# Performance work log

Hardware: AMD Instinct MI355X
Metric: run time of the kernel (lower is better)

## Reference

```python
import jax, jax.numpy as jnp
import numpy as np

EPS = 1e-6
D = 512      # embedding_dim
M = 4        # n_modules
B = 4        # batch
S = 128      # seq_len
K = 32       # stack_size
STEPS = 16   # max_steps (ACT)
SCALE = D ** (-0.5)


def _clin(zr, zi, Wr, Wi, sub):
    # complex linear: (Wr + i Wi)(zr + i zi), torch Linear convention y = x @ W.T
    yr = jnp.einsum(sub, zr, Wr) - jnp.einsum(sub, zi, Wi)
    yi = jnp.einsum(sub, zi, Wr) + jnp.einsum(sub, zr, Wi)
    return yr, yi


def forward_fn(x_real, x_imag, Wl_r, Wl_i, Wq_r, Wq_i, Wk_r, Wk_i, Wv_r, Wv_i,
               ln_scale, ln_shift, mod_bias, gate_mask,
               score_w, score_b, conf_w, conf_b, halt_w, halt_b,
               ctrl_w, ctrl_b, st_score_w, st_score_b, st_conf_w, st_conf_b):
    mem0 = jnp.zeros((B, K, 2 * D), x_real.dtype)
    ptr0 = jnp.zeros((B, K), x_real.dtype).at[:, 0].set(1.0)
    acc0 = jnp.zeros((B, S, 2 * D), x_real.dtype)
    rem0 = jnp.ones((B,), x_real.dtype)

    def step(carry, _):
        sr, si, mem, ptr, acc, rem = carry
        # ComplexAttentionBlock (all M modules vectorized on axis m)
        cr = 0.5 * x_real + 0.5 * sr
        ci = 0.5 * x_imag + 0.5 * si
        zr, zi = _clin(cr, ci, Wl_r, Wl_i, 'bsd,mod->bmso')   # [B,M,S,D]
        # ComplexLayerNorm (magnitude LN, unbiased var as torch.var default)
        mag = jnp.sqrt(zr * zr + zi * zi) + EPS
        mean = mag.mean(-1, keepdims=True)
        var = mag.var(-1, keepdims=True, ddof=1)
        nm = (mag - mean) / jnp.sqrt(var + EPS)
        nm = nm * ln_scale[None, :, None, :] + ln_shift[None, :, None, :]
        ph = jnp.arctan2(zi, zr)
        zr = nm * jnp.cos(ph)
        zi = nm * jnp.sin(ph)
        # ModReLU
        nrm = jnp.sqrt(zr * zr + zi * zi) + EPS
        sc = jax.nn.relu(nrm + mod_bias[None, :, None, :]) / nrm
        zr = zr * sc
        zi = zi * sc
        # ComplexAttention over concatenated real/imag q,k
        sub = 'bmsd,mod->bmso'
        qr, qi = _clin(zr, zi, Wq_r, Wq_i, sub)
        kr, ki = _clin(zr, zi, Wk_r, Wk_i, sub)
        vr, vi = _clin(zr, zi, Wv_r, Wv_i, sub)
        qf = jnp.concatenate([qr, qi], -1)   # [B,M,S,2D]
        kf = jnp.concatenate([kr, ki], -1)
        attn = jax.nn.softmax(jnp.einsum('bmse,bmte->bmst', qf, kf) * SCALE, axis=-1)
        ar = jnp.einsum('bmst,bmtd->bmsd', attn, vr)
        ai = jnp.einsum('bmst,bmtd->bmsd', attn, vi)
        # SigmoidGatingMask
        g = jax.nn.sigmoid(gate_mask)[None, :, None, :]
        pr = ar * g
        pi = ai * g
        flat = jnp.concatenate([pr, pi], -1)  # [B,M,S,2D]
        score = jnp.einsum('bmse,me->bms', flat, score_w) + score_b[None, :, None]
        conf = jax.nn.sigmoid(jnp.einsum('bmse,me->bms', flat, conf_w) + conf_b[None, :, None])
        halt = jnp.einsum('bmse,me->bms', flat, halt_w) + halt_b[None, :, None]
        # DifferentiableStack on seq-pooled broadcast state
        flat_in = jnp.concatenate([sr.mean(1), si.mean(1)], -1)  # [B,2D]
        control = jax.nn.softmax(flat_in @ ctrl_w + ctrl_b, axis=-1)  # [B,3]
        push, pop, noop = control[:, 0:1], control[:, 1:2], control[:, 2:3]
        ptr_up = jnp.roll(ptr, 1, axis=1)
        ptr_dn = jnp.roll(ptr, -1, axis=1)
        new_ptr = push * ptr_up + pop * ptr_dn + noop * ptr
        new_ptr = new_ptr / (new_ptr.sum(1, keepdims=True) + EPS)
        wmask = push * ptr_up                                   # [B,K]
        new_mem = wmask[..., None] * flat_in[:, None, :] + mem * (1.0 - wmask[..., None])
        read = (new_mem * new_ptr[..., None]).sum(1)            # [B,2D]
        sp_r, sp_i = read[:, :D], read[:, D:]
        st_sc = read @ st_score_w + st_score_b[0]               # [B]
        st_cf = jax.nn.sigmoid(read @ st_conf_w + st_conf_b[0])
        # combine M block proposals + stack proposal via score*confidence softmax
        all_pr = jnp.concatenate([pr, jnp.broadcast_to(sp_r[:, None, None, :], (B, 1, S, D))], 1)
        all_pi = jnp.concatenate([pi, jnp.broadcast_to(sp_i[:, None, None, :], (B, 1, S, D))], 1)
        all_sc = jnp.concatenate([score, jnp.broadcast_to(st_sc[:, None, None], (B, 1, S))], 1)
        all_cf = jnp.concatenate([conf, jnp.broadcast_to(st_cf[:, None, None], (B, 1, S))], 1)
        w = jax.nn.softmax(all_sc * all_cf, axis=1)[..., None]  # [B,M+1,S,1]
        new_sr = (w * all_pr).sum(1)
        new_si = (w * all_pi).sum(1)
        # ACT halting accumulation
        p = jax.nn.sigmoid(halt).mean(axis=(1, 2))              # [B]
        acc = acc + (p * rem)[:, None, None] * jnp.concatenate([new_sr, new_si], -1)
        rem = rem * (1.0 - p)
        return (new_sr, new_si, new_mem, new_ptr, acc, rem), None

    carry, _ = jax.lax.scan(step, (x_real, x_imag, mem0, ptr0, acc0, rem0), None, length=STEPS)
    sr, si, _, _, acc, rem = carry
    # add ACT remainder weight on final state
    out = acc + rem[:, None, None] * jnp.concatenate([sr, si], -1)
    return out  # [B,S,2D] real/imag concat


def setup_inputs() -> dict:
    key = jax.random.key(0)
    ks = jax.random.split(key, 24)
    w = 1.0 / np.sqrt(D)
    h = 0.02
    inp = {
        'x_real': jax.random.normal(ks[0], (B, S, D), jnp.float32),
        'x_imag': jax.random.normal(ks[1], (B, S, D), jnp.float32),
        'Wl_r': jax.random.normal(ks[2], (M, D, D), jnp.float32) * w,
        'Wl_i': jax.random.normal(ks[3], (M, D, D), jnp.float32) * w,
        'Wq_r': jax.random.normal(ks[4], (M, D, D), jnp.float32) * w,
        'Wq_i': jax.random.normal(ks[5], (M, D, D), jnp.float32) * w,
        'Wk_r': jax.random.normal(ks[6], (M, D, D), jnp.float32) * w,
        'Wk_i': jax.random.normal(ks[7], (M, D, D), jnp.float32) * w,
        'Wv_r': jax.random.normal(ks[8], (M, D, D), jnp.float32) * w,
        'Wv_i': jax.random.normal(ks[9], (M, D, D), jnp.float32) * w,
        'ln_scale': jnp.ones((M, D), jnp.float32),
        'ln_shift': jnp.zeros((M, D), jnp.float32),
        'mod_bias': jnp.zeros((M, D), jnp.float32),
        'gate_mask': jnp.ones((M, D), jnp.float32),
        'score_w': jax.random.normal(ks[10], (M, 2 * D), jnp.float32) * h,
        'score_b': jnp.zeros((M,), jnp.float32),
        'conf_w': jax.random.normal(ks[11], (M, 2 * D), jnp.float32) * h,
        'conf_b': jnp.zeros((M,), jnp.float32),
        'halt_w': jax.random.normal(ks[12], (M, 2 * D), jnp.float32) * h,
        'halt_b': jnp.full((M,), -4.0, jnp.float32),  # nn.init.constant_(halt_head.bias, -4.0)
        'ctrl_w': jax.random.normal(ks[13], (2 * D, 3), jnp.float32) * h,
        'ctrl_b': jnp.zeros((3,), jnp.float32),
        'st_score_w': jax.random.normal(ks[14], (2 * D,), jnp.float32) * h,
        'st_score_b': jnp.zeros((1,), jnp.float32),
        'st_conf_w': jax.random.normal(ks[15], (2 * D,), jnp.float32) * h,
        'st_conf_b': jnp.zeros((1,), jnp.float32),
    }
    return inp


def reference(x_real, x_imag, Wl_r, Wl_i, Wq_r, Wq_i, Wk_r, Wk_i, Wv_r, Wv_i,
              ln_scale, ln_shift, mod_bias, gate_mask,
              score_w, score_b, conf_w, conf_b, halt_w, halt_b,
              ctrl_w, ctrl_b, st_score_w, st_score_b, st_conf_w, st_conf_b):
    return forward_fn(x_real, x_imag, Wl_r, Wl_i, Wq_r, Wq_i, Wk_r, Wk_i, Wv_r, Wv_i,
                      ln_scale, ln_shift, mod_bias, gate_mask,
                      score_w, score_b, conf_w, conf_b, halt_w, halt_b,
                      ctrl_w, ctrl_b, st_score_w, st_score_b, st_conf_w, st_conf_b)
```

## Files before the change

kernel.cpp:

```cpp
#include <hip/hip_runtime.h>

#define DD 512
#define MM 4
#define BB 4
#define SS 128
#define KK 32
#define NSTEPS 16
#define EPSF 1e-6f
#define SCALEF 0.04419417382415922f

typedef unsigned short u16;
typedef __bf16 bf16x8 __attribute__((ext_vector_type(8)));
typedef u16 u16x8 __attribute__((ext_vector_type(8)));
typedef float f32x16 __attribute__((ext_vector_type(16)));
typedef unsigned int u32x4 __attribute__((ext_vector_type(4)));

__device__ inline void split_bf16(float x, u16& h, u16& l) {
  __bf16 hb = (__bf16)x;
  float hf = (float)hb;
  __bf16 lb = (__bf16)(x - hf);
  h = __builtin_bit_cast(u16, hb);
  l = __builtin_bit_cast(u16, lb);
}

__global__ void k_convw(const float* __restrict__ src, u16* __restrict__ dst) {
  int idx = blockIdx.x * 256 + threadIdx.x;
  int row = idx >> 9, k = idx & 511;
  u16 h, l;
  split_bf16(src[idx], h, l);
  dst[(size_t)row * 1024 + k] = h;
  dst[(size_t)row * 1024 + 512 + k] = l;
}

__global__ void k_convt(const float* __restrict__ src, u16* __restrict__ dst) {
  __shared__ float tile[64][65];
  int m = blockIdx.z;
  int o0 = blockIdx.y * 64, d0 = blockIdx.x * 64;
  int tid = threadIdx.x;
  int g = tid >> 6, lane = tid & 63;
#pragma unroll
  for (int i = 0; i < 16; i++) {
    int o_l = g * 16 + i;
// ... 93 lines not shown
    ctrl[0] = e0 / s; ctrl[1] = e1 / s; ctrl[2] = e2 / s;
    stacc[b * 2] = 0.f; stacc[b * 2 + 1] = 0.f;
  }
  __syncthreads();
  if (tid < KK) {
    float up = optr[(tid + KK - 1) & (KK - 1)];
    float dn = optr[(tid + 1) & (KK - 1)];
    float cu = optr[tid];
    nptr_s[tid] = ctrl[0] * up + ctrl[1] * dn + ctrl[2] * cu;
    wm_s[tid] = ctrl[0] * up;
  }
  __syncthreads();
  if (tid == 0) {
    float s = 0.f;
    for (int k = 0; k < KK; k++) s += nptr_s[k];
    normf = 1.f / (s + EPSF);
  }
  __syncthreads();
  if (tid < KK) {
    float np = nptr_s[tid] * normf;
    ptrv[b * KK + tid] = np;
    nptrg[b * KK + tid] = np;
    wmg[b * KK + tid] = wm_s[tid];
  }
}

#define LSTR 72

__global__ __launch_bounds__(256) void k_gemm_mfma(
    const u16* __restrict__ Ar, const u16* __restrict__ Ai,
    const u16* __restrict__ Wr, const u16* __restrict__ Wi,
    float* __restrict__ Cr, float* __restrict__ Ci) {
  __shared__ u16 sAr[64][LSTR], sAi[64][LSTR], sWr[64][LSTR], sWi[64][LSTR];
  int m = blockIdx.z;
  int row_blk = blockIdx.y * 64, o_blk = blockIdx.x * 64;
  int tid = threadIdx.x;

  int lrow = tid >> 3, lk8 = (tid & 7) << 3;
  size_t arow0 = (size_t)(row_blk + lrow), arow1 = arow0 + 32;
  size_t wrow0 = (size_t)m * DD + o_blk + lrow, wrow1 = wrow0 + 32;

  int wave = tid >> 6, lane = tid & 63;
  int wrow = (wave >> 1) * 32, wcol = (wave & 1) * 32;
  int l31 = lane & 31, khalf = (lane >> 5) * 8;

  f32x16 accP, accN, accI;
  for (int i = 0; i < 16; i++) { accP[i] = 0.f; accN[i] = 0.f; accI[i] = 0.f; }

  u16x8 g0 = *(const u16x8*)&Ar[arow0 * 1024 + lk8];
  u16x8 g1 = *(const u16x8*)&Ar[arow1 * 1024 + lk8];
  u16x8 g2 = *(const u16x8*)&Ai[arow0 * 1024 + lk8];
  u16x8 g3 = *(const u16x8*)&Ai[arow1 * 1024 + lk8];
  u16x8 g4 = *(const u16x8*)&Wr[wrow0 * 1024 + lk8];
  u16x8 g5 = *(const u16x8*)&Wr[wrow1 * 1024 + lk8];
  u16x8 g6 = *(const u16x8*)&Wi[wrow0 * 1024 + lk8];
  u16x8 g7 = *(const u16x8*)&Wi[wrow1 * 1024 + lk8];

  for (int it = 0; it < 24; ++it) {
    __syncthreads();
    *(u16x8*)&sAr[lrow][lk8] = g0;
    *(u16x8*)&sAr[lrow + 32][lk8] = g1;
    *(u16x8*)&sAi[lrow][lk8] = g2;
    *(u16x8*)&sAi[lrow + 32][lk8] = g3;
    *(u16x8*)&sWr[lrow][lk8] = g4;
    *(u16x8*)&sWr[lrow + 32][lk8] = g5;
    *(u16x8*)&sWi[lrow][lk8] = g6;
    *(u16x8*)&sWi[lrow + 32][lk8] = g7;
    u16x8 n0, n1, n2, n3, n4, n5, n6, n7;
    if (it < 23) {
      int it2 = it + 1, seg = it2 >> 3, k0 = (it2 & 7) * 64;
      int aofs = (seg == 1) ? 512 : 0, wofs = (seg == 2) ? 512 : 0;
      n0 = *(const u16x8*)&Ar[arow0 * 1024 + aofs + k0 + lk8];
      n1 = *(const u16x8*)&Ar[arow1 * 1024 + aofs + k0 + lk8];
      n2 = *(const u16x8*)&Ai[arow0 * 1024 + aofs + k0 + lk8];
      n3 = *(const u16x8*)&Ai[arow1 * 1024 + aofs + k0 + lk8];
      n4 = *(const u16x8*)&Wr[wrow0 * 1024 + wofs + k0 + lk8];
      n5 = *(const u16x8*)&Wr[wrow1 * 1024 + wofs + k0 + lk8];
      n6 = *(const u16x8*)&Wi[wrow0 * 1024 + wofs + k0 + lk8];
      n7 = *(const u16x8*)&Wi[wrow1 * 1024 + wofs + k0 + lk8];
    }
    __syncthreads();
#pragma unroll
    for (int kk = 0; kk < 64; kk += 16) {
      bf16x8 fAr = *(const bf16x8*)&sAr[wrow + l31][kk + khalf];
      bf16x8 fAi = *(const bf16x8*)&sAi[wrow + l31][kk + khalf];
      bf16x8 fWr = *(const bf16x8*)&sWr[wcol + l31][kk + khalf];
      bf16x8 fWi = *(const bf16x8*)&sWi[wcol + l31][kk + khalf];
      accP = __builtin_amdgcn_mfma_f32_32x32x16_bf16(fAr, fWr, accP, 0, 0, 0);
      accN = __builtin_amdgcn_mfma_f32_32x32x16_bf16(fAi, fWi, accN, 0, 0, 0);
      accI = __builtin_amdgcn_mfma_f32_32x32x16_bf16(fAi, fWr, accI, 0, 0, 0);
      accI = __builtin_amdgcn_mfma_f32_32x32x16_bf16(fAr, fWi, accI, 0, 0, 0);
    }
    if (it < 23) {
      g0 = n0; g1 = n1; g2 = n2; g3 = n3; g4 = n4; g5 = n5; g6 = n6; g7 = n7;
    }
  }

  int o = o_blk + wcol + l31;
#pragma unroll
  for (int reg = 0; reg < 16; reg++) {
    int r_in = (reg & 3) + 8 * (reg >> 2) + 4 * (lane >> 5);
    int gr = row_blk + wrow + r_in;
    int b = gr >> 7, s = gr & (SS - 1);
    size_t crow = (size_t)((b * MM + m) * SS + s);
    Cr[crow * DD + o] = accP[reg] - accN[reg];
    Ci[crow * DD + o] = accI[reg];
  }
}

__global__ __launch_bounds__(256) void k_gemm_g(
    const u16* __restrict__ Ar, const u16* __restrict__ Ai,
    const u16* __restrict__ Wr, const u16* __restrict__ Wi,
    float* __restrict__ Hr, float* __restrict__ Hi) {
  __shared__ u16 sAr[64][LSTR], sAi[64][LSTR], sWr[64][LSTR], sWi[64][LSTR];
  int m = blockIdx.z;
  int row_blk = blockIdx.y * 64, o_blk = blockIdx.x * 64;
  int tid = threadIdx.x;

  int lrow = tid >> 3, lk8 = (tid & 7) << 3;
  size_t arow0 = (size_t)(m * 512 + row_blk + lrow), arow1 = arow0 + 32;
  size_t wrow0 = (size_t)(m * 512 + o_blk + lrow), wrow1 = wrow0 + 32;

  int wave = tid >> 6, lane = tid & 63;
  int wrow = (wave >> 1) * 32, wcol = (wave & 1) * 32;
  int l31 = lane & 31, khalf = (lane >> 5) * 8;

  f32x16 accP, accN, accI;
  for (int i = 0; i < 16; i++) { accP[i] = 0.f; accN[i] = 0.f; accI[i] = 0.f; }

  u16x8 g0 = *(const u16x8*)&Ar[arow0 * 1024 + lk8];
  u16x8 g1 = *(const u16x8*)&Ar[arow1 * 1024 + lk8];
  u16x8 g2 = *(const u16x8*)&Ai[arow0 * 1024 + lk8];
  u16x8 g3 = *(const u16x8*)&Ai[arow1 * 1024 + lk8];
  u16x8 g4 = *(const u16x8*)&Wr[wrow0 * 1024 + lk8];
  u16x8 g5 = *(const u16x8*)&Wr[wrow1 * 1024 + lk8];
  u16x8 g6 = *(const u16x8*)&Wi[wrow0 * 1024 + lk8];
  u16x8 g7 = *(const u16x8*)&Wi[wrow1 * 1024 + lk8];

  for (int it = 0; it < 24; ++it) {
    __syncthreads();
    *(u16x8*)&sAr[lrow][lk8] = g0;
    *(u16x8*)&sAr[lrow + 32][lk8] = g1;
    *(u16x8*)&sAi[lrow][lk8] = g2;
    *(u16x8*)&sAi[lrow + 32][lk8] = g3;
    *(u16x8*)&sWr[lrow][lk8] = g4;
    *(u16x8*)&sWr[lrow + 32][lk8] = g5;
    *(u16x8*)&sWi[lrow][lk8] = g6;
    *(u16x8*)&sWi[lrow + 32][lk8] = g7;
    u16x8 n0, n1, n2, n3, n4, n5, n6, n7;
    if (it < 23) {
      int it2 = it + 1, seg = it2 >> 3, k0 = (it2 & 7) * 64;
      int aofs = (seg == 1) ? 512 : 0, wofs = (seg == 2) ? 512 : 0;
      n0 = *(const u16x8*)&Ar[arow0 * 1024 + aofs + k0 + lk8];
      n1 = *(const u16x8*)&Ar[arow1 * 1024 + aofs + k0 + lk8];
      n2 = *(const u16x8*)&Ai[arow0 * 1024 + aofs + k0 + lk8];
      n3 = *(const u16x8*)&Ai[arow1 * 1024 + aofs + k0 + lk8];
      n4 = *(const u16x8*)&Wr[wrow0 * 1024 + wofs + k0 + lk8];
      n5 = *(const u16x8*)&Wr[wrow1 * 1024 + wofs + k0 + lk8];
      n6 = *(const u16x8*)&Wi[wrow0 * 1024 + wofs + k0 + lk8];
      n7 = *(const u16x8*)&Wi[wrow1 * 1024 + wofs + k0 + lk8];
    }
    __syncthreads();
#pragma unroll
    for (int kk = 0; kk < 64; kk += 16) {
      bf16x8 fAr = *(const bf16x8*)&sAr[wrow + l31][kk + khalf];
      bf16x8 fAi = *(const bf16x8*)&sAi[wrow + l31][kk + khalf];
      bf16x8 fWr = *(const bf16x8*)&sWr[wcol + l31][kk + khalf];
      bf16x8 fWi = *(const bf16x8*)&sWi[wcol + l31][kk + khalf];
      u32x4 t = __builtin_bit_cast(u32x4, fAi) ^ 0x80008000u;
      bf16x8 nAi = __builtin_bit_cast(bf16x8, t);
      accP = __builtin_amdgcn_mfma_f32_32x32x16_bf16(fAr, fWr, accP, 0, 0, 0);
      accN = __builtin_amdgcn_mfma_f32_32x32x16_bf16(fAi, fWi, accN, 0, 0, 0);
      accI = __builtin_amdgcn_mfma_f32_32x32x16_bf16(fAr, fWi, accI, 0, 0, 0);
      accI = __builtin_amdgcn_mfma_f32_32x32x16_bf16(nAi, fWr, accI, 0, 0, 0);
    }
    if (it < 23) {
      g0 = n0; g1 = n1; g2 = n2; g3 = n3; g4 = n4; g5 = n5; g6 = n6; g7 = n7;
    }
  }

  int o = o_blk + wcol + l31;
#pragma unroll
  for (int reg = 0; reg < 16; reg++) {
    int r_in = (reg & 3) + 8 * (reg >> 2) + 4 * (lane >> 5);
    int gr = row_blk + wrow + r_in;
    size_t crow = (size_t)(m * 512 + gr);
    Hr[crow * DD + o] = accP[reg] + accN[reg];
    Hi[crow * DD + o] = accI[reg];
  }
}

__global__ __launch_bounds__(256) void k_gemm_qkv(
    const u16* __restrict__ Ar, const u16* __restrict__ Ai,
    const u16* __restrict__ wbf, size_t WSLOT,
    u16* __restrict__ qbr, u16* __restrict__ qbi,
    u16* __restrict__ vbr, u16* __restrict__ vbi) {
  __shared__ u16 sAr[64][LSTR], sAi[64][LSTR], sWr[64][LSTR], sWi[64][LSTR];
  int zid = blockIdx.z;
  int m = zid >> 1, w = zid & 1;
  int slot = (w == 0) ? 8 : 6;
  const u16* Wr = wbf + (size_t)slot * WSLOT;
  const u16* Wi = Wr + WSLOT;
  int row_blk = blockIdx.y * 64, o_blk = blockIdx.x * 64;
  int tid = threadIdx.x;

  int lrow = tid >> 3, lk8 = (tid & 7) << 3;
  int gr0 = row_blk + lrow, gr1 = gr0 + 32;
  size_t arow0 = (size_t)(((gr0 >> 7) * MM + m) * SS + (gr0 & (SS - 1)));
  size_t arow1 = (size_t)(((gr1 >> 7) * MM + m) * SS + (gr1 & (SS - 1)));
  size_t wrow0 = (size_t)m * DD + o_blk + lrow, wrow1 = wrow0 + 32;

  int wave = tid >> 6, lane = tid & 63;
  int wrow = (wave >> 1) * 32, wcol = (wave & 1) * 32;
  int l31 = lane & 31, khalf = (lane >> 5) * 8;

  f32x16 accP, accN, accI;
  for (int i = 0; i < 16; i++) { accP[i] = 0.f; accN[i] = 0.f; accI[i] = 0.f; }

  u16x8 g0 = *(const u16x8*)&Ar[arow0 * 1024 + lk8];
  u16x8 g1 = *(const u16x8*)&Ar[arow1 * 1024 + lk8];
  u16x8 g2 = *(const u16x8*)&Ai[arow0 * 1024 + lk8];
  u16x8 g3 = *(const u16x8*)&Ai[arow1 * 1024 + lk8];
  u16x8 g4 = *(const u16x8*)&Wr[wrow0 * 1024 + lk8];
  u16x8 g5 = *(const u16x8*)&Wr[wrow1 * 1024 + lk8];
  u16x8 g6 = *(const u16x8*)&Wi[wrow0 * 1024 + lk8];
  u16x8 g7 = *(const u16x8*)&Wi[wrow1 * 1024 + lk8];

  for (int it = 0; it < 24; ++it) {
    __syncthreads();
    *(u16x8*)&sAr[lrow][lk8] = g0;
    *(u16x8*)&sAr[lrow + 32][lk8] = g1;
    *(u16x8*)&sAi[lrow][lk8] = g2;
    *(u16x8*)&sAi[lrow + 32][lk8] = g3;
    *(u16x8*)&sWr[lrow][lk8] = g4;
    *(u16x8*)&sWr[lrow + 32][lk8] = g5;
    *(u16x8*)&sWi[lrow][lk8] = g6;
    *(u16x8*)&sWi[lrow + 32][lk8] = g7;
    u16x8 n0, n1, n2, n3, n4, n5, n6, n7;
    if (it < 23) {
      int it2 = it + 1, seg = it2 >> 3, k0 = (it2 & 7) * 64;
      int aofs = (seg == 1) ? 512 : 0, wofs = (seg == 2) ? 512 : 0;
      n0 = *(const u16x8*)&Ar[arow0 * 1024 + aofs + k0 + lk8];
      n1 = *(const u16x8*)&Ar[arow1 * 1024 + aofs + k0 + lk8];
      n2 = *(const u16x8*)&Ai[arow0 * 1024 + aofs + k0 + lk8];
      n3 = *(const u16x8*)&Ai[arow1 * 1024 + aofs + k0 + lk8];
      n4 = *(const u16x8*)&Wr[wrow0 * 1024 + wofs + k0 + lk8];
      n5 = *(const u16x8*)&Wr[wrow1 * 1024 + wofs + k0 + lk8];
      n6 = *(const u16x8*)&Wi[wrow0 * 1024 + wofs + k0 + lk8];
      n7 = *(const u16x8*)&Wi[wrow1 * 1024 + wofs + k0 + lk8];
    }
    __syncthreads();
#pragma unroll
    for (int kk = 0; kk < 64; kk += 16) {
      bf16x8 fAr = *(const bf16x8*)&sAr[wrow + l31][kk + khalf];
      bf16x8 fAi = *(const bf16x8*)&sAi[wrow + l31][kk + khalf];
      bf16x8 fWr = *(const bf16x8*)&sWr[wcol + l31][kk + khalf];
      bf16x8 fWi = *(const bf16x8*)&sWi[wcol + l31][kk + khalf];
      accP = __builtin_amdgcn_mfma_f32_32x32x16_bf16(fAr, fWr, accP, 0, 0, 0);
      accN = __builtin_amdgcn_mfma_f32_32x32x16_bf16(fAi, fWi, accN, 0, 0, 0);
      accI = __builtin_amdgcn_mfma_f32_32x32x16_bf16(fAi, fWr, accI, 0, 0, 0);
      accI = __builtin_amdgcn_mfma_f32_32x32x16_bf16(fAr, fWi, accI, 0, 0, 0);
    }
    if (it < 23) {
      g0 = n0; g1 = n1; g2 = n2; g3 = n3; g4 = n4; g5 = n5; g6 = n6; g7 = n7;
    }
  }

  u16* Cr = (w == 0) ? qbr : vbr;
  u16* Ci = (w == 0) ? qbi : vbi;
  int o = o_blk + wcol + l31;
#pragma unroll
  for (int reg = 0; reg < 16; reg++) {
    int r_in = (reg & 3) + 8 * (reg >> 2) + 4 * (lane >> 5);
    int gr = row_blk + wrow + r_in;
    int b = gr >> 7, s = gr & (SS - 1);
    size_t crow = (size_t)((b * MM + m) * SS + s);
    u16 h, l;
    split_bf16(accP[reg] - accN[reg], h, l);
    Cr[crow * 1024 + o] = h;
    Cr[crow * 1024 + 512 + o] = l;
    split_bf16(accI[reg], h, l);
    Ci[crow * 1024 + o] = h;
    Ci[crow * 1024 + 512 + o] = l;
  }
}

__global__ __launch_bounds__(256) void k_scores_sm(
    const u16* __restrict__ Q_r, const u16* __restrict__ Q_i,
    const u16* __restrict__ K_r, const u16* __restrict__ K_i,
    u16* __restrict__ Pb) {
  __shared__ __align__(16) char smem[55296];
  u16 (*sQr)[LSTR] = (u16(*)[LSTR])smem;
  u16 (*sQi)[LSTR] = (u16(*)[LSTR])(smem + 9216);
  u16 (*sKr)[LSTR] = (u16(*)[LSTR])(smem + 18432);
  u16 (*sKi)[LSTR] = (u16(*)[LSTR])(smem + 36864);
  float (*stile)[132] = (float(*)[132])smem;

  int bm = blockIdx.z;
  int s_blk = blockIdx.y * 64;
  int tid = threadIdx.x;
  int lrow = tid >> 3, lk8 = (tid & 7) << 3;
  size_t qrow0 = (size_t)(bm * SS + s_blk + lrow), qrow1 = qrow0 + 32;
  size_t krow = (size_t)(bm * SS + lrow);

  int wave = tid >> 6, lane = tid & 63;
  int srow_w = (wave & 1) * 32;
  int tcol_w = (wave >> 1) * 64;
  int l31 = lane & 31, khalf = (lane >> 5) * 8;

  f32x16 acc0, acc1;
  for (int i = 0; i < 16; i++) { acc0[i] = 0.f; acc1[i] = 0.f; }

  for (int it = 0; it < 24; ++it) {
    int seg = it >> 3, k0 = (it & 7) * 64;
    int qofs = (seg == 1) ? 512 : 0;
    int kofs = (seg == 2) ? 512 : 0;
    u16x8 q0 = *(const u16x8*)&Q_r[qrow0 * 1024 + qofs + k0 + lk8];
    u16x8 q1 = *(const u16x8*)&Q_r[qrow1 * 1024 + qofs + k0 + lk8];
    u16x8 q2 = *(const u16x8*)&Q_i[qrow0 * 1024 + qofs + k0 + lk8];
    u16x8 q3 = *(const u16x8*)&Q_i[qrow1 * 1024 + qofs + k0 + lk8];
    u16x8 kr0 = *(const u16x8*)&K_r[(krow + 0) * 1024 + kofs + k0 + lk8];
    u16x8 kr1 = *(const u16x8*)&K_r[(krow + 32) * 1024 + kofs + k0 + lk8];
    u16x8 kr2 = *(const u16x8*)&K_r[(krow + 64) * 1024 + kofs + k0 + lk8];
    u16x8 kr3 = *(const u16x8*)&K_r[(krow + 96) * 1024 + kofs + k0 + lk8];
    u16x8 ki0 = *(const u16x8*)&K_i[(krow + 0) * 1024 + kofs + k0 + lk8];
    u16x8 ki1 = *(const u16x8*)&K_i[(krow + 32) * 1024 + kofs + k0 + lk8];
    u16x8 ki2 = *(const u16x8*)&K_i[(krow + 64) * 1024 + kofs + k0 + lk8];
    u16x8 ki3 = *(const u16x8*)&K_i[(krow + 96) * 1024 + kofs + k0 + lk8];
    __syncthreads();
    *(u16x8*)&sQr[lrow][lk8] = q0;
    *(u16x8*)&sQr[lrow + 32][lk8] = q1;
    *(u16x8*)&sQi[lrow][lk8] = q2;
    *(u16x8*)&sQi[lrow + 32][lk8] = q3;
    *(u16x8*)&sKr[lrow][lk8] = kr0;
    *(u16x8*)&sKr[lrow + 32][lk8] = kr1;
    *(u16x8*)&sKr[lrow + 64][lk8] = kr2;
    *(u16x8*)&sKr[lrow + 96][lk8] = kr3;
    *(u16x8*)&sKi[lrow][lk8] = ki0;
    *(u16x8*)&sKi[lrow + 32][lk8] = ki1;
    *(u16x8*)&sKi[lrow + 64][lk8] = ki2;
    *(u16x8*)&sKi[lrow + 96][lk8] = ki3;
    __syncthreads();
#pragma unroll
    for (int kk = 0; kk < 64; kk += 16) {
      bf16x8 fQr = *(const bf16x8*)&sQr[srow_w + l31][kk + khalf];
      bf16x8 fQi = *(const bf16x8*)&sQi[srow_w + l31][kk + khalf];
      bf16x8 fKr0 = *(const bf16x8*)&sKr[tcol_w + l31][kk + khalf];
      bf16x8 fKr1 = *(const bf16x8*)&sKr[tcol_w + 32 + l31][kk + khalf];
      bf16x8 fKi0 = *(const bf16x8*)&sKi[tcol_w + l31][kk + khalf];
      bf16x8 fKi1 = *(const bf16x8*)&sKi[tcol_w + 32 + l31][kk + khalf];
      acc0 = __builtin_amdgcn_mfma_f32_32x32x16_bf16(fQr, fKr0, acc0, 0, 0, 0);
      acc0 = __builtin_amdgcn_mfma_f32_32x32x16_bf16(fQi, fKi0, acc0, 0, 0, 0);
      acc1 = __builtin_amdgcn_mfma_f32_32x32x16_bf16(fQr, fKr1, acc1, 0, 0, 0);
      acc1 = __builtin_amdgcn_mfma_f32_32x32x16_bf16(fQi, fKi1, acc1, 0, 0, 0);
    }
  }

  __syncthreads();
#pragma unroll
  for (int reg = 0; reg < 16; reg++) {
    int r = srow_w + (reg & 3) + 8 * (reg >> 2) + 4 * (lane >> 5);
    stile[r][tcol_w + l31] = acc0[reg] * SCALEF;
    stile[r][tcol_w + 32 + l31] = acc1[reg] * SCALEF;
  }
  __syncthreads();
  int row = tid >> 2;
  int quarter = tid & 3;
  float mx = -3.4e38f;
#pragma unroll
  for (int j = 0; j < 32; j++) mx = fmaxf(mx, stile[row][quarter * 32 + j]);
  mx = fmaxf(mx, __shfl_xor(mx, 1));
  mx = fmaxf(mx, __shfl_xor(mx, 2));
  float ev[32];
  float sum = 0.f;
#pragma unroll
  for (int j = 0; j < 32; j++) {
    ev[j] = expf(stile[row][quarter * 32 + j] - mx);
    sum += ev[j];
  }
  sum += __shfl_xor(sum, 1);
  sum += __shfl_xor(sum, 2);
  float inv = 1.f / sum;
  size_t prow = (size_t)(bm * SS + s_blk + row) * 256;
#pragma unroll
  for (int j = 0; j < 32; j++) {
    int c = quarter * 32 + j;
    u16 h, l;
// ... 72 lines not shown
    float vR = accR[reg] * g, vI = accI[reg] * g;
    pr[crow * DD + d] = vR;
    pi[crow * DD + d] = vI;
    float ps = vR * swr + vI * swi;
    float pc = vR * cwr + vI * cwi;
    float ph = vR * hwr + vI * hwi;
#pragma unroll
    for (int off = 1; off < 32; off <<= 1) {
      ps += __shfl_xor(ps, off);
      pc += __shfl_xor(pc, off);
      ph += __shfl_xor(ph, off);
    }
    if (l31 == 0) {
      atomicAdd(&scorev[crow], ps);
      atomicAdd(&confv[crow], pc);
      atomicAdd(&haltv[crow], ph);
    }
  }
}

__global__ void k_lnphase(const float* __restrict__ zr, const float* __restrict__ zi,
                          const float* __restrict__ ln_scale, const float* __restrict__ ln_shift,
                          const float* __restrict__ mod_bias,
                          u16* __restrict__ zbr, u16* __restrict__ zbi) {
  int row = blockIdx.x;
  int m = (row >> 7) & (MM - 1);
  int tid = threadIdx.x;
  size_t base = (size_t)row * DD;
  float zrv[4], ziv[4], rv[4];
  float sum = 0.f, sumsq = 0.f;
#pragma unroll
  for (int i = 0; i < 4; i++) {
    int o = tid + i * 128;
    float a = zr[base + o], bv = zi[base + o];
    zrv[i] = a; ziv[i] = bv;
    float r = sqrtf(a * a + bv * bv);
    rv[i] = r;
    float mg = r + EPSF;
    sum += mg;
    sumsq += mg * mg;
  }
  __shared__ float rs[128], rq[128];
  rs[tid] = sum; rq[tid] = sumsq;
  __syncthreads();
  for (int off = 64; off > 0; off >>= 1) {
    if (tid < off) { rs[tid] += rs[tid + off]; rq[tid] += rq[tid + off]; }
    __syncthreads();
  }
  float mean = rs[0] * (1.0f / DD);
  float var = (rq[0] - (float)DD * mean * mean) * (1.0f / (DD - 1));
  float inv = 1.0f / sqrtf(var + EPSF);
#pragma unroll
  for (int i = 0; i < 4; i++) {
    int o = tid + i * 128;
    float mg = rv[i] + EPSF;
    float nm = (mg - mean) * inv * ln_scale[m * DD + o] + ln_shift[m * DD + o];
    float r = rv[i];
    float cosp, sinp;
    if (r > 0.f) { cosp = zrv[i] / r; sinp = ziv[i] / r; }
    else { cosp = 1.f; sinp = 0.f; }
    float z1r = nm * cosp, z1i = nm * sinp;
    float nrm = sqrtf(z1r * z1r + z1i * z1i) + EPSF;
    float sc = fmaxf(nrm + mod_bias[m * DD + o], 0.f) / nrm;
    u16 h, l;
    split_bf16(z1r * sc, h, l);
    zbr[(size_t)row * 1024 + o] = h;
    zbr[(size_t)row * 1024 + 512 + o] = l;
// ... 134 lines not shown

extern "C" void kernel_launch(void* const* d_in, const int* in_sizes, int n_in,
                              void* d_out, int out_size, void* d_ws, size_t ws_size,
                              hipStream_t stream) {
  const float* xr = (const float*)d_in[0];
  const float* xi = (const float*)d_in[1];
  const float* Wl_r = (const float*)d_in[2];
  const float* Wl_i = (const float*)d_in[3];
  const float* Wq_r = (const float*)d_in[4];
  const float* Wq_i = (const float*)d_in[5];
  const float* Wk_r = (const float*)d_in[6];
  const float* Wk_i = (const float*)d_in[7];
  const float* Wv_r = (const float*)d_in[8];
  const float* Wv_i = (const float*)d_in[9];
  const float* ln_scale = (const float*)d_in[10];
  const float* ln_shift = (const float*)d_in[11];
  const float* mod_bias = (const float*)d_in[12];
  const float* gate_mask = (const float*)d_in[13];
  const float* score_w = (const float*)d_in[14];
  const float* score_b = (const float*)d_in[15];
  const float* conf_w = (const float*)d_in[16];
  const float* conf_b = (const float*)d_in[17];
  const float* halt_w = (const float*)d_in[18];
  const float* halt_b = (const float*)d_in[19];
  const float* ctrl_w = (const float*)d_in[20];
  const float* ctrl_b = (const float*)d_in[21];
  const float* st_score_w = (const float*)d_in[22];
  const float* st_score_b = (const float*)d_in[23];
  const float* st_conf_w = (const float*)d_in[24];
  const float* st_conf_b = (const float*)d_in[25];
  float* out = (float*)d_out;

  const int BSD = BB * SS * DD;
  const int BMSD = BB * MM * SS * DD;
  const size_t WSLOT = (size_t)MM * DD * 1024;

  char* pc = (char*)d_ws;
  float* sr = (float*)pc; pc += (size_t)BSD * 4;
  float* si = (float*)pc; pc += (size_t)BSD * 4;
  float* zr = (float*)pc; pc += (size_t)BMSD * 4;
  float* zi = (float*)pc; pc += (size_t)BMSD * 4;
  float* prb = (float*)pc; pc += (size_t)BMSD * 4;
  float* pib = (float*)pc; pc += (size_t)BMSD * 4;
  float* scorev = (float*)pc; pc += (size_t)BB * MM * SS * 4;
  float* confv = (float*)pc; pc += (size_t)BB * MM * SS * 4;
  float* haltv = (float*)pc; pc += (size_t)BB * MM * SS * 4;
  float* flat = (float*)pc; pc += (size_t)BB * 2 * DD * 4;
  float* stacc = (float*)pc; pc += 64;
  float* nptrg = (float*)pc; pc += (size_t)BB * KK * 4;
  float* wmg = (float*)pc; pc += (size_t)BB * KK * 4;
  float* memv = (float*)pc; pc += (size_t)BB * KK * 2 * DD * 4;
  float* ptrv = (float*)pc; pc += (size_t)BB * KK * 4;
  float* readv = (float*)pc; pc += (size_t)BB * 2 * DD * 4;
  float* stv = (float*)pc; pc += (size_t)2 * BB * 4;
  float* accb = (float*)pc; pc += (size_t)BB * SS * 2 * DD * 4;
  float* rem = (float*)pc; pc += (size_t)BB * 4;
  float* coeff = (float*)pc; pc += (size_t)BB * 4;
  u16* crbf = (u16*)pc; pc += (size_t)BB * SS * 1024 * 2;
  u16* cibf = (u16*)pc; pc += (size_t)BB * SS * 1024 * 2;
  u16* zbr = (u16*)pc; pc += (size_t)BB * MM * SS * 1024 * 2;
  u16* zbi = (u16*)pc; pc += (size_t)BB * MM * SS * 1024 * 2;
  u16* qbr = (u16*)pc; pc += (size_t)BB * MM * SS * 1024 * 2;
  u16* qbi = (u16*)pc; pc += (size_t)BB * MM * SS * 1024 * 2;
  u16* vbr = (u16*)pc; pc += (size_t)BB * MM * SS * 1024 * 2;
  u16* vbi = (u16*)pc; pc += (size_t)BB * MM * SS * 1024 * 2;
  u16* Pb  = (u16*)pc; pc += (size_t)BB * MM * SS * 256 * 2;
  u16* wbf = (u16*)pc; pc += 10 * WSLOT * 2;
  u16* wqtr = (u16*)pc; pc += WSLOT * 2;
  u16* wqti = (u16*)pc; pc += WSLOT * 2;
  u16* wktr = (u16*)pc; pc += WSLOT * 2;
  u16* wkti = (u16*)pc; pc += WSLOT * 2;
  float* hfr = (float*)pc; pc += (size_t)MM * DD * DD * 4;
  float* hfi = (float*)pc; pc += (size_t)MM * DD * DD * 4;

  k_convw<<<4096, 256, 0, stream>>>(Wl_r, wbf + 0 * WSLOT);
  k_convw<<<4096, 256, 0, stream>>>(Wl_i, wbf + 1 * WSLOT);
  k_convw<<<4096, 256, 0, stream>>>(Wv_r, wbf + 6 * WSLOT);
  k_convw<<<4096, 256, 0, stream>>>(Wv_i, wbf + 7 * WSLOT);

  dim3 tgrid(8, 8, 4);
  k_convt<<<tgrid, 256, 0, stream>>>(Wq_r, wqtr);
  k_convt<<<tgrid, 256, 0, stream>>>(Wq_i, wqti);
  k_convt<<<tgrid, 256, 0, stream>>>(Wk_r, wktr);
  k_convt<<<tgrid, 256, 0, stream>>>(Wk_i, wkti);

  dim3 hgrid(8, 8, 4);
  k_gemm_g<<<hgrid, 256, 0, stream>>>(wktr, wkti, wqtr, wqti, hfr, hfi);
  k_convw<<<4096, 256, 0, stream>>>(hfr, wbf + 8 * WSLOT);
  k_convw<<<4096, 256, 0, stream>>>(hfi, wbf + 9 * WSLOT);

  k_init<<<2048, 256, 0, stream>>>(xr, xi, sr, si, accb, memv, ptrv, rem, crbf, cibf);

  dim3 ggrid(DD / 64, (BB * SS) / 64, MM);
  dim3 qgrid(DD / 64, (BB * SS) / 64, MM * 2);
  dim3 smgrid(1, SS / 64, BB * MM);
  dim3 pvgrid(DD / 64, SS / 64, BB * MM);

  for (int step = 0; step < NSTEPS; ++step) {
    k_flatctrl<<<BB, 256, 0, stream>>>(sr, si, ctrl_w, ctrl_b, ptrv, flat, nptrg, wmg, stacc,
                                       scorev, confv, haltv);
    k_gemm_mfma<<<ggrid, 256, 0, stream>>>(crbf, cibf, wbf + 0 * WSLOT, wbf + 1 * WSLOT, zr, zi);
    k_lnphase<<<BB * MM * SS, 128, 0, stream>>>(zr, zi, ln_scale, ln_shift, mod_bias, zbr, zbi);
    k_gemm_qkv<<<qgrid, 256, 0, stream>>>(zbr, zbi, wbf, WSLOT, qbr, qbi, vbr, vbi);
    k_scores_sm<<<smgrid, 256, 0, stream>>>(qbr, qbi, zbr, zbi, Pb);
    k_pv<<<pvgrid, 256, 0, stream>>>(Pb, vbr, vbi, gate_mask, score_w, conf_w, halt_w,
                                     prb, pib, scorev, confv, haltv);
    k_memup<<<BB * 4, 256, 0, stream>>>(flat, nptrg, wmg, memv, readv,
                                        st_score_w, st_conf_w, stacc);
    k_haltp<<<BB, 256, 0, stream>>>(haltv, halt_b, rem, coeff, stacc, st_score_b, st_conf_b, stv);
    k_combine<<<BB * SS, 256, 0, stream>>>(prb, pib, scorev, confv, score_b, conf_b,
                                           stv, readv, coeff,
                                           xr, xi, sr, si, accb, crbf, cibf);
  }

  k_final<<<(BB * SS * 2 * DD) / 256, 256, 0, stream>>>(accb, rem, sr, si, out);
}
```

Baseline: 2.273 ms.

## Split-K the first complex GEMM in two and prefetch score-kernel tiles

The first complex linear GEMM now splits its 24 K-iterations into two interleaved halves across twice as many blocks. Each half writes a partial result to its own buffer, and the layer-norm kernel sums the two. This doubles the grid from 256 to 512 blocks to fill more CUs, at the cost of extra fp32 writes and reads of the partials. Separately, the scores kernel now register-prefetches the next Q/K tile, so global loads overlap with the MFMA work instead of stalling before each shared-memory store.

```diff
diff --git a/kernel.cpp b/kernel.cpp
--- a/kernel.cpp
+++ b/kernel.cpp
@@ -8,6 +8,7 @@
 #define NSTEPS 16
 #define EPSF 1e-6f
 #define SCALEF 0.04419417382415922f
+#define BMSD (BB * MM * SS * DD)
 
 typedef unsigned short u16;
 typedef __bf16 bf16x8 __attribute__((ext_vector_type(8)));
@@ -167,13 +168,104 @@
     const u16* __restrict__ Wr, const u16* __restrict__ Wi,
     float* __restrict__ Cr, float* __restrict__ Ci) {
   __shared__ u16 sAr[64][LSTR], sAi[64][LSTR], sWr[64][LSTR], sWi[64][LSTR];
-  int m = blockIdx.z;
+  int mz = blockIdx.z;
+  int m = mz & (MM - 1), split = mz >> 2;
   int row_blk = blockIdx.y * 64, o_blk = blockIdx.x * 64;
   int tid = threadIdx.x;
 
   int lrow = tid >> 3, lk8 = (tid & 7) << 3;
   size_t arow0 = (size_t)(row_blk + lrow), arow1 = arow0 + 32;
   size_t wrow0 = (size_t)m * DD + o_blk + lrow, wrow1 = wrow0 + 32;
+
+  int wave = tid >> 6, lane = tid & 63;
+  int wrow = (wave >> 1) * 32, wcol = (wave & 1) * 32;
+  int l31 = lane & 31, khalf = (lane >> 5) * 8;
+
+  f32x16 accP, accN, accI;
+  for (int i = 0; i < 16; i++) { accP[i] = 0.f; accN[i] = 0.f; accI[i] = 0.f; }
+
+  {
+    int it2 = split, seg = it2 >> 3, k0 = (it2 & 7) * 64;
+    int aofs = (seg == 1) ? 512 : 0, wofs = (seg == 2) ? 512 : 0;
+    (void)aofs; (void)wofs;
+  }
+  int it20 = split;
+  int seg0 = it20 >> 3, k00 = (it20 & 7) * 64;
+  int aofs0 = (seg0 == 1) ? 512 : 0, wofs0 = (seg0 == 2) ? 512 : 0;
+  u16x8 g0 = *(const u16x8*)&Ar[arow0 * 1024 + aofs0 + k00 + lk8];
+  u16x8 g1 = *(const u16x8*)&Ar[arow1 * 1024 + aofs0 + k00 + lk8];
+  u16x8 g2 = *(const u16x8*)&Ai[arow0 * 1024 + aofs0 + k00 + lk8];
+  u16x8 g3 = *(const u16x8*)&Ai[arow1 * 1024 + aofs0 + k00 + lk8];
+  u16x8 g4 = *(const u16x8*)&Wr[wrow0 * 1024 + wofs0 + k00 + lk8];
+  u16x8 g5 = *(const u16x8*)&Wr[wrow1 * 1024 + wofs0 + k00 + lk8];
+  u16x8 g6 = *(const u16x8*)&Wi[wrow0 * 1024 + wofs0 + k00 + lk8];
+  u16x8 g7 = *(const u16x8*)&Wi[wrow1 * 1024 + wofs0 + k00 + lk8];
+
+  for (int jt = 0; jt < 12; ++jt) {
+    __syncthreads();
+    *(u16x8*)&sAr[lrow][lk8] = g0;
+    *(u16x8*)&sAr[lrow + 32][lk8] = g1;
+    *(u16x8*)&sAi[lrow][lk8] = g2;
+    *(u16x8*)&sAi[lrow + 32][lk8] = g3;
+    *(u16x8*)&sWr[lrow][lk8] = g4;
+    *(u16x8*)&sWr[lrow + 32][lk8] = g5;
+    *(u16x8*)&sWi[lrow][lk8] = g6;
+    *(u16x8*)&sWi[lrow + 32][lk8] = g7;
+    u16x8 n0, n1, n2, n3, n4, n5, n6, n7;
+    if (jt < 11) {
+      int it2 = 2 * (jt + 1) + split, seg = it2 >> 3, k0 = (it2 & 7) * 64;
+      int aofs = (seg == 1) ? 512 : 0, wofs = (seg == 2) ? 512 : 0;
+      n0 = *(const u16x8*)&Ar[arow0 * 1024 + aofs + k0 + lk8];
+      n1 = *(const u16x8*)&Ar[arow1 * 1024 + aofs + k0 + lk8];
+      n2 = *(const u16x8*)&Ai[arow0 * 1024 + aofs + k0 + lk8];
+      n3 = *(const u16x8*)&Ai[arow1 * 1024 + aofs + k0 + lk8];
+      n4 = *(const u16x8*)&Wr[wrow0 * 1024 + wofs + k0 + lk8];
+      n5 = *(const u16x8*)&Wr[wrow1 * 1024 + wofs + k0 + lk8];
+      n6 = *(const u16x8*)&Wi[wrow0 * 1024 + wofs + k0 + lk8];
+      n7 = *(const u16x8*)&Wi[wrow1 * 1024 + wofs + k0 + lk8];
+    }
+    __syncthreads();
+#pragma unroll
+    for (int kk = 0; kk < 64; kk += 16) {
+      bf16x8 fAr = *(const bf16x8*)&sAr[wrow + l31][kk + khalf];
+      bf16x8 fAi = *(const bf16x8*)&sAi[wrow + l31][kk + khalf];
+      bf16x8 fWr = *(const bf16x8*)&sWr[wcol + l31][kk + khalf];
+      bf16x8 fWi = *(const bf16x8*)&sWi[wcol + l31][kk + khalf];
+      accP = __builtin_amdgcn_mfma_f32_32x32x16_bf16(fAr, fWr, accP, 0, 0, 0);
+      accN = __builtin_amdgcn_mfma_f32_32x32x16_bf16(fAi, fWi, accN, 0, 0, 0);
+      accI = __builtin_amdgcn_mfma_f32_32x32x16_bf16(fAi, fWr, accI, 0, 0, 0);
+      accI = __builtin_amdgcn_mfma_f32_32x32x16_bf16(fAr, fWi, accI, 0, 0, 0);
+    }
+    if (jt < 11) {
+      g0 = n0; g1 = n1; g2 = n2; g3 = n3; g4 = n4; g5 = n5; g6 = n6; g7 = n7;
+    }
+  }
+
+  int o = o_blk + wcol + l31;
+  size_t sofs = (size_t)split * BMSD;
+#pragma unroll
+  for (int reg = 0; reg < 16; reg++) {
+    int r_in = (reg & 3) + 8 * (reg >> 2) + 4 * (lane >> 5);
+    int gr = row_blk + wrow + r_in;
+    int b = gr >> 7, s = gr & (SS - 1);
+    size_t crow = (size_t)((b * MM + m) * SS + s);
+    Cr[sofs + crow * DD + o] = accP[reg] - accN[reg];
+    Ci[sofs + crow * DD + o] = accI[reg];
+  }
+}
+
+__global__ __launch_bounds__(256) void k_gemm_g(
+    const u16* __restrict__ Ar, const u16* __restrict__ Ai,
+    const u16* __restrict__ Wr, const u16* __restrict__ Wi,
+    float* __restrict__ Hr, float* __restrict__ Hi) {
+  __shared__ u16 sAr[64][LSTR], sAi[64][LSTR], sWr[64][LSTR], sWi[64][LSTR];
+  int m = blockIdx.z;
+  int row_blk = blockIdx.y * 64, o_blk = blockIdx.x * 64;
+  int tid = threadIdx.x;
+
+  int lrow = tid >> 3, lk8 = (tid & 7) << 3;
+  size_t arow0 = (size_t)(m * 512 + row_blk + lrow), arow1 = arow0 + 32;
+  size_t wrow0 = (size_t)(m * 512 + o_blk + lrow), wrow1 = wrow0 + 32;
 
   int wave = tid >> 6, lane = tid & 63;
   int wrow = (wave >> 1) * 32, wcol = (wave & 1) * 32;
@@ -221,10 +313,12 @@
       bf16x8 fAi = *(const bf16x8*)&sAi[wrow + l31][kk + khalf];
       bf16x8 fWr = *(const bf16x8*)&sWr[wcol + l31][kk + khalf];
       bf16x8 fWi = *(const bf16x8*)&sWi[wcol + l31][kk + khalf];
+      u32x4 t = __builtin_bit_cast(u32x4, fAi) ^ 0x80008000u;
+      bf16x8 nAi = __builtin_bit_cast(bf16x8, t);
       accP = __builtin_amdgcn_mfma_f32_32x32x16_bf16(fAr, fWr, accP, 0, 0, 0);
       accN = __builtin_amdgcn_mfma_f32_32x32x16_bf16(fAi, fWi, accN, 0, 0, 0);
-      accI = __builtin_amdgcn_mfma_f32_32x32x16_bf16(fAi, fWr, accI, 0, 0, 0);
       accI = __builtin_amdgcn_mfma_f32_32x32x16_bf16(fAr, fWi, accI, 0, 0, 0);
+      accI = __builtin_amdgcn_mfma_f32_32x32x16_bf16(nAi, fWr, accI, 0, 0, 0);
     }
     if (it < 23) {
       g0 = n0; g1 = n1; g2 = n2; g3 = n3; g4 = n4; g5 = n5; g6 = n6; g7 = n7;
@@ -236,25 +330,31 @@
   for (int reg = 0; reg < 16; reg++) {
     int r_in = (reg & 3) + 8 * (reg >> 2) + 4 * (lane >> 5);
     int gr = row_blk + wrow + r_in;
-    int b = gr >> 7, s = gr & (SS - 1);
-    size_t crow = (size_t)((b * MM + m) * SS + s);
-    Cr[crow * DD + o] = accP[reg] - accN[reg];
-    Ci[crow * DD + o] = accI[reg];
-  }
-}
-
-__global__ __launch_bounds__(256) void k_gemm_g(
+    size_t crow = (size_t)(m * 512 + gr);
+    Hr[crow * DD + o] = accP[reg] + accN[reg];
+    Hi[crow * DD + o] = accI[reg];
+  }
+}
+
+__global__ __launch_bounds__(256) void k_gemm_qkv(
     const u16* __restrict__ Ar, const u16* __restrict__ Ai,
-    const u16* __restrict__ Wr, const u16* __restrict__ Wi,
-    float* __restrict__ Hr, float* __restrict__ Hi) {
+    const u16* __restrict__ wbf, size_t WSLOT,
+    u16* __restrict__ qbr, u16* __restrict__ qbi,
+    u16* __restrict__ vbr, u16* __restrict__ vbi) {
   __shared__ u16 sAr[64][LSTR], sAi[64][LSTR], sWr[64][LSTR], sWi[64][LSTR];
-  int m = blockIdx.z;
+  int zid = blockIdx.z;
+  int m = zid >> 1, w = zid & 1;
+  int slot = (w == 0) ? 8 : 6;
+  const u16* Wr = wbf + (size_t)slot * WSLOT;
+  const u16* Wi = Wr + WSLOT;
   int row_blk = blockIdx.y * 64, o_blk = blockIdx.x * 64;
   int tid = threadIdx.x;
 
   int lrow = tid >> 3, lk8 = (tid & 7) << 3;
-  size_t arow0 = (size_t)(m * 512 + row_blk + lrow), arow1 = arow0 + 32;
-  size_t wrow0 = (size_t)(m * 512 + o_blk + lrow), wrow1 = wrow0 + 32;
+  int gr0 = row_blk + lrow, gr1 = gr0 + 32;
+  size_t arow0 = (size_t)(((gr0 >> 7) * MM + m) * SS + (gr0 & (SS - 1)));
+  size_t arow1 = (size_t)(((gr1 >> 7) * MM + m) * SS + (gr1 & (SS - 1)));
+  size_t wrow0 = (size_t)m * DD + o_blk + lrow, wrow1 = wrow0 + 32;
 
   int wave = tid >> 6, lane = tid & 63;
   int wrow = (wave >> 1) * 32, wcol = (wave & 1) * 32;
@@ -302,95 +402,6 @@
       bf16x8 fAi = *(const bf16x8*)&sAi[wrow + l31][kk + khalf];
       bf16x8 fWr = *(const bf16x8*)&sWr[wcol + l31][kk + khalf];
       bf16x8 fWi = *(const bf16x8*)&sWi[wcol + l31][kk + khalf];
-      u32x4 t = __builtin_bit_cast(u32x4, fAi) ^ 0x80008000u;
-      bf16x8 nAi = __builtin_bit_cast(bf16x8, t);
-      accP = __builtin_amdgcn_mfma_f32_32x32x16_bf16(fAr, fWr, accP, 0, 0, 0);
-      accN = __builtin_amdgcn_mfma_f32_32x32x16_bf16(fAi, fWi, accN, 0, 0, 0);
-      accI = __builtin_amdgcn_mfma_f32_32x32x16_bf16(fAr, fWi, accI, 0, 0, 0);
-      accI = __builtin_amdgcn_mfma_f32_32x32x16_bf16(nAi, fWr, accI, 0, 0, 0);
-    }
-    if (it < 23) {
-      g0 = n0; g1 = n1; g2 = n2; g3 = n3; g4 = n4; g5 = n5; g6 = n6; g7 = n7;
-    }
-  }
-
-  int o = o_blk + wcol + l31;
-#pragma unroll
-  for (int reg = 0; reg < 16; reg++) {
-    int r_in = (reg & 3) + 8 * (reg >> 2) + 4 * (lane >> 5);
-    int gr = row_blk + wrow + r_in;
-    size_t crow = (size_t)(m * 512 + gr);
-    Hr[crow * DD + o] = accP[reg] + accN[reg];
-    Hi[crow * DD + o] = accI[reg];
-  }
-}
-
-__global__ __launch_bounds__(256) void k_gemm_qkv(
-    const u16* __restrict__ Ar, const u16* __restrict__ Ai,
-    const u16* __restrict__ wbf, size_t WSLOT,
-    u16* __restrict__ qbr, u16* __restrict__ qbi,
-    u16* __restrict__ vbr, u16* __restrict__ vbi) {
-  __shared__ u16 sAr[64][LSTR], sAi[64][LSTR], sWr[64][LSTR], sWi[64][LSTR];
-  int zid = blockIdx.z;
-  int m = zid >> 1, w = zid & 1;
-  int slot = (w == 0) ? 8 : 6;
-  const u16* Wr = wbf + (size_t)slot * WSLOT;
-  const u16* Wi = Wr + WSLOT;
-  int row_blk = blockIdx.y * 64, o_blk = blockIdx.x * 64;
-  int tid = threadIdx.x;
-
-  int lrow = tid >> 3, lk8 = (tid & 7) << 3;
-  int gr0 = row_blk + lrow, gr1 = gr0 + 32;
-  size_t arow0 = (size_t)(((gr0 >> 7) * MM + m) * SS + (gr0 & (SS - 1)));
-  size_t arow1 = (size_t)(((gr1 >> 7) * MM + m) * SS + (gr1 & (SS - 1)));
-  size_t wrow0 = (size_t)m * DD + o_blk + lrow, wrow1 = wrow0 + 32;
-
-  int wave = tid >> 6, lane = tid & 63;
-  int wrow = (wave >> 1) * 32, wcol = (wave & 1) * 32;
-  int l31 = lane & 31, khalf = (lane >> 5) * 8;
-
-  f32x16 accP, accN, accI;
-  for (int i = 0; i < 16; i++) { accP[i] = 0.f; accN[i] = 0.f; accI[i] = 0.f; }
-
-  u16x8 g0 = *(const u16x8*)&Ar[arow0 * 1024 + lk8];
-  u16x8 g1 = *(const u16x8*)&Ar[arow1 * 1024 + lk8];
-  u16x8 g2 = *(const u16x8*)&Ai[arow0 * 1024 + lk8];
-  u16x8 g3 = *(const u16x8*)&Ai[arow1 * 1024 + lk8];
-  u16x8 g4 = *(const u16x8*)&Wr[wrow0 * 1024 + lk8];
-  u16x8 g5 = *(const u16x8*)&Wr[wrow1 * 1024 + lk8];
-  u16x8 g6 = *(const u16x8*)&Wi[wrow0 * 1024 + lk8];
-  u16x8 g7 = *(const u16x8*)&Wi[wrow1 * 1024 + lk8];
-
-  for (int it = 0; it < 24; ++it) {
-    __syncthreads();
-    *(u16x8*)&sAr[lrow][lk8] = g0;
-    *(u16x8*)&sAr[lrow + 32][lk8] = g1;
-    *(u16x8*)&sAi[lrow][lk8] = g2;
-    *(u16x8*)&sAi[lrow + 32][lk8] = g3;
-    *(u16x8*)&sWr[lrow][lk8] = g4;
-    *(u16x8*)&sWr[lrow + 32][lk8] = g5;
-    *(u16x8*)&sWi[lrow][lk8] = g6;
-    *(u16x8*)&sWi[lrow + 32][lk8] = g7;
-    u16x8 n0, n1, n2, n3, n4, n5, n6, n7;
-    if (it < 23) {
-      int it2 = it + 1, seg = it2 >> 3, k0 = (it2 & 7) * 64;
-      int aofs = (seg == 1) ? 512 : 0, wofs = (seg == 2) ? 512 : 0;
-      n0 = *(const u16x8*)&Ar[arow0 * 1024 + aofs + k0 + lk8];
-      n1 = *(const u16x8*)&Ar[arow1 * 1024 + aofs + k0 + lk8];
-      n2 = *(const u16x8*)&Ai[arow0 * 1024 + aofs + k0 + lk8];
-      n3 = *(const u16x8*)&Ai[arow1 * 1024 + aofs + k0 + lk8];
-      n4 = *(const u16x8*)&Wr[wrow0 * 1024 + wofs + k0 + lk8];
-      n5 = *(const u16x8*)&Wr[wrow1 * 1024 + wofs + k0 + lk8];
-      n6 = *(const u16x8*)&Wi[wrow0 * 1024 + wofs + k0 + lk8];
-      n7 = *(const u16x8*)&Wi[wrow1 * 1024 + wofs + k0 + lk8];
-    }
-    __syncthreads();
-#pragma unroll
-    for (int kk = 0; kk < 64; kk += 16) {
-      bf16x8 fAr = *(const bf16x8*)&sAr[wrow + l31][kk + khalf];
-      bf16x8 fAi = *(const bf16x8*)&sAi[wrow + l31][kk + khalf];
-      bf16x8 fWr = *(const bf16x8*)&sWr[wcol + l31][kk + khalf];
-      bf16x8 fWi = *(const bf16x8*)&sWi[wcol + l31][kk + khalf];
       accP = __builtin_amdgcn_mfma_f32_32x32x16_bf16(fAr, fWr, accP, 0, 0, 0);
       accN = __builtin_amdgcn_mfma_f32_32x32x16_bf16(fAi, fWi, accN, 0, 0, 0);
       accI = __builtin_amdgcn_mfma_f32_32x32x16_bf16(fAi, fWr, accI, 0, 0, 0);
@@ -446,35 +457,43 @@
   f32x16 acc0, acc1;
   for (int i = 0; i < 16; i++) { acc0[i] = 0.f; acc1[i] = 0.f; }
 
+  u16x8 pf[12];
+  pf[0] = *(const u16x8*)&Q_r[qrow0 * 1024 + lk8];
+  pf[1] = *(const u16x8*)&Q_r[qrow1 * 1024 + lk8];
+  pf[2] = *(const u16x8*)&Q_i[qrow0 * 1024 + lk8];
+  pf[3] = *(const u16x8*)&Q_i[qrow1 * 1024 + lk8];
+#pragma unroll
+  for (int q = 0; q < 4; q++) {
+    pf[4 + q] = *(const u16x8*)&K_r[(krow + q * 32) * 1024 + lk8];
+    pf[8 + q] = *(const u16x8*)&K_i[(krow + q * 32) * 1024 + lk8];
+  }
+
   for (int it = 0; it < 24; ++it) {
-    int seg = it >> 3, k0 = (it & 7) * 64;
-    int qofs = (seg == 1) ? 512 : 0;
-    int kofs = (seg == 2) ? 512 : 0;
-    u16x8 q0 = *(const u16x8*)&Q_r[qrow0 * 1024 + qofs + k0 + lk8];
-    u16x8 q1 = *(const u16x8*)&Q_r[qrow1 * 1024 + qofs + k0 + lk8];
-    u16x8 q2 = *(const u16x8*)&Q_i[qrow0 * 1024 + qofs + k0 + lk8];
-    u16x8 q3 = *(const u16x8*)&Q_i[qrow1 * 1024 + qofs + k0 + lk8];
-    u16x8 kr0 = *(const u16x8*)&K_r[(krow + 0) * 1024 + kofs + k0 + lk8];
-    u16x8 kr1 = *(const u16x8*)&K_r[(krow + 32) * 1024 + kofs + k0 + lk8];
-    u16x8 kr2 = *(const u16x8*)&K_r[(krow + 64) * 1024 + kofs + k0 + lk8];
-    u16x8 kr3 = *(const u16x8*)&K_r[(krow + 96) * 1024 + kofs + k0 + lk8];
-    u16x8 ki0 = *(const u16x8*)&K_i[(krow + 0) * 1024 + kofs + k0 + lk8];
-    u16x8 ki1 = *(const u16x8*)&K_i[(krow + 32) * 1024 + kofs + k0 + lk8];
-    u16x8 ki2 = *(const u16x8*)&K_i[(krow + 64) * 1024 + kofs + k0 + lk8];
-    u16x8 ki3 = *(const u16x8*)&K_i[(krow + 96) * 1024 + kofs + k0 + lk8];
-    __syncthreads();
-    *(u16x8*)&sQr[lrow][lk8] = q0;
-    *(u16x8*)&sQr[lrow + 32][lk8] = q1;
-    *(u16x8*)&sQi[lrow][lk8] = q2;
-    *(u16x8*)&sQi[lrow + 32][lk8] = q3;
-    *(u16x8*)&sKr[lrow][lk8] = kr0;
-    *(u16x8*)&sKr[lrow + 32][lk8] = kr1;
-    *(u16x8*)&sKr[lrow + 64][lk8] = kr2;
-    *(u16x8*)&sKr[lrow + 96][lk8] = kr3;
-    *(u16x8*)&sKi[lrow][lk8] = ki0;
-    *(u16x8*)&sKi[lrow + 32][lk8] = ki1;
-    *(u16x8*)&sKi[lrow + 64][lk8] = ki2;
-    *(u16x8*)&sKi[lrow + 96][lk8] = ki3;
+    __syncthreads();
+    *(u16x8*)&sQr[lrow][lk8] = pf[0];
+    *(u16x8*)&sQr[lrow + 32][lk8] = pf[1];
+    *(u16x8*)&sQi[lrow][lk8] = pf[2];
+    *(u16x8*)&sQi[lrow + 32][lk8] = pf[3];
+#pragma unroll
+    for (int q = 0; q < 4; q++) {
+      *(u16x8*)&sKr[lrow + q * 32][lk8] = pf[4 + q];
+      *(u16x8*)&sKi[lrow + q * 32][lk8] = pf[8 + q];
+    }
+    u16x8 nf[12];
+    if (it < 23) {
+      int it2 = it + 1, seg = it2 >> 3, k0 = (it2 & 7) * 64;
+      int qofs = (seg == 1) ? 512 : 0;
+      int kofs = (seg == 2) ? 512 : 0;
+      nf[0] = *(const u16x8*)&Q_r[qrow0 * 1024 + qofs + k0 + lk8];
+      nf[1] = *(const u16x8*)&Q_r[qrow1 * 1024 + qofs + k0 + lk8];
+      nf[2] = *(const u16x8*)&Q_i[qrow0 * 1024 + qofs + k0 + lk8];
+      nf[3] = *(const u16x8*)&Q_i[qrow1 * 1024 + qofs + k0 + lk8];
+#pragma unroll
+      for (int q = 0; q < 4; q++) {
+        nf[4 + q] = *(const u16x8*)&K_r[(krow + q * 32) * 1024 + kofs + k0 + lk8];
+        nf[8 + q] = *(const u16x8*)&K_i[(krow + q * 32) * 1024 + kofs + k0 + lk8];
+      }
+    }
     __syncthreads();
 #pragma unroll
     for (int kk = 0; kk < 64; kk += 16) {
@@ -488,6 +507,10 @@
       acc0 = __builtin_amdgcn_mfma_f32_32x32x16_bf16(fQi, fKi0, acc0, 0, 0, 0);
       acc1 = __builtin_amdgcn_mfma_f32_32x32x16_bf16(fQr, fKr1, acc1, 0, 0, 0);
       acc1 = __builtin_amdgcn_mfma_f32_32x32x16_bf16(fQi, fKi1, acc1, 0, 0, 0);
+    }
+    if (it < 23) {
+#pragma unroll
+      for (int j = 0; j < 12; j++) pf[j] = nf[j];
     }
   }
 
@@ -626,7 +649,8 @@
 #pragma unroll
   for (int i = 0; i < 4; i++) {
     int o = tid + i * 128;
-    float a = zr[base + o], bv = zi[base + o];
+    float a = zr[base + o] + zr[(size_t)BMSD + base + o];
+    float bv = zi[base + o] + zi[(size_t)BMSD + base + o];
     zrv[i] = a; ziv[i] = bv;
     float r = sqrtf(a * a + bv * bv);
     rv[i] = r;
@@ -827,14 +851,13 @@
   float* out = (float*)d_out;
 
   const int BSD = BB * SS * DD;
-  const int BMSD = BB * MM * SS * DD;
   const size_t WSLOT = (size_t)MM * DD * 1024;
 
   char* pc = (char*)d_ws;
   float* sr = (float*)pc; pc += (size_t)BSD * 4;
   float* si = (float*)pc; pc += (size_t)BSD * 4;
-  float* zr = (float*)pc; pc += (size_t)BMSD * 4;
-  float* zi = (float*)pc; pc += (size_t)BMSD * 4;
+  float* zr = (float*)pc; pc += (size_t)2 * BMSD * 4;
+  float* zi = (float*)pc; pc += (size_t)2 * BMSD * 4;
   float* prb = (float*)pc; pc += (size_t)BMSD * 4;
   float* pib = (float*)pc; pc += (size_t)BMSD * 4;
   float* scorev = (float*)pc; pc += (size_t)BB * MM * SS * 4;
@@ -886,7 +909,7 @@
 
   k_init<<<2048, 256, 0, stream>>>(xr, xi, sr, si, accb, memv, ptrv, rem, crbf, cibf);
 
-  dim3 ggrid(DD / 64, (BB * SS) / 64, MM);
+  dim3 ggrid(DD / 64, (BB * SS) / 64, MM * 2);
   dim3 qgrid(DD / 64, (BB * SS) / 64, MM * 2);
   dim3 smgrid(1, SS / 64, BB * MM);
   dim3 pvgrid(DD / 64, SS / 64, BB * MM);
```

Result: faster. 2.186 ms (-3.9%).
